# Performance work log

Measured on AMD Instinct MI355X. Metric: run time of the kernel, lower is better.

## Reference

```python
import jax, jax.numpy as jnp
import numpy as np

BIN_AGG = 2  # binAgg in binFunc

def pair_mean(x):
    # mean over non-overlapping groups of BIN_AGG along last dim, then repeat back
    B, C, H, W = x.shape
    m = x.reshape(B, C, H, W // BIN_AGG, BIN_AGG).mean(axis=-1)  # [B,C,H,W/2]
    return jnp.repeat(m, BIN_AGG, axis=-1)  # [B,C,H,W]

def bin_active(x):
    # binFunc(x, abs_bin=True) * sign(x): per-pair mean of |x| carrying the sign of x
    return pair_mean(jnp.abs(x)) * jnp.sign(x)

def setup_inputs() -> dict:
    key = jax.random.key(0)
    k1, k2, k3 = jax.random.split(key, 3)
    Cin, Cout, K = 256, 256, 3
    x = jax.random.normal(k1, (32, Cin, 56, 56), jnp.float32)
    bound = 1.0 / np.sqrt(Cin * K * K)  # torch Conv2d default init range
    weight = jax.random.uniform(k2, (Cout, Cin, K, K), jnp.float32, -bound, bound)
    bias = jax.random.uniform(k3, (Cout,), jnp.float32, -bound, bound)
    return {"x": x, "weight": weight, "bias": bias}

def reference(x, weight, bias):
    xb = bin_active(x)
    out = jax.lax.conv_general_dilated(
        xb, weight, window_strides=(1, 1), padding=[(1, 1), (1, 1)],
        dimension_numbers=("NCHW", "OIHW", "NCHW"))
    return out + bias[None, :, None, None]
```

## Files before the change

kernel.cpp:

```cpp
#include <hip/hip_runtime.h>
#include <hip/hip_bf16.h>
#include <cstdint>

typedef unsigned short u16;
typedef __attribute__((ext_vector_type(8))) short short8;
typedef __attribute__((ext_vector_type(8))) unsigned short ushort8;
typedef __attribute__((ext_vector_type(4))) float f32x4;

#define NB   32
#define CIN  256
#define HH   56
#define WWID 56
#define HP   58
#define WP   58
#define COUT 256
#define NSPAT (NB*HH*WWID)

__device__ __forceinline__ u16 f2bf(float f) {
  uint32_t u = __float_as_uint(f);
  u += 0x7FFFu + ((u >> 16) & 1u);
  return (u16)(u >> 16);
}

__device__ __forceinline__ void gload16(const void* g, void* lds) {
  auto* gp = reinterpret_cast<const __attribute__((address_space(1))) uint32_t*>(
      reinterpret_cast<uintptr_t>(g));
  auto* lp = reinterpret_cast<__attribute__((address_space(3))) uint32_t*>(
      reinterpret_cast<uintptr_t>(lds));
  __builtin_amdgcn_global_load_lds(gp, lp, 16, 0, 0);
}

__global__ __launch_bounds__(256) void prep_x_kernel(const float* __restrict__ x,
                                                     u16* __restrict__ xbp) {
  const int n = blockIdx.x, hp = blockIdx.y, t = threadIdx.x;
  u16* row = xbp + ((size_t)(n*HP + hp))*WP*CIN;
  if (hp == 0 || hp == HP-1) {
    uint32_t* p = (uint32_t*)row;
    for (int i = t; i < WP*CIN/2; i += 256) p[i] = 0;
    return;
  }
  const int h = hp - 1;
  __shared__ u16 lds[HH*CIN];
  if (t < 224) {
    const int f4 = t % 14, cg = t / 14;
    const int sw = f4 & 7;
    #pragma unroll
    for (int it = 0; it < 2; it++) {
      const int c8 = it*16 + cg;
      const int c0 = c8 * 8;
      const float* xc = x + (((size_t)n*CIN + c0)*HH + h)*WWID + f4*4;
      float4 v[8];
      #pragma unroll
      for (int r = 0; r < 8; r++) v[r] = *(const float4*)(xc + (size_t)r*HH*WWID);
      u16 o[8][4];
      #pragma unroll
      for (int r = 0; r < 8; r++) {
        const float m01 = 0.5f*(fabsf(v[r].x)+fabsf(v[r].y));
        const float m23 = 0.5f*(fabsf(v[r].z)+fabsf(v[r].w));
        o[r][0] = f2bf(v[r].x == 0.f ? 0.f : copysignf(m01, v[r].x));
        o[r][1] = f2bf(v[r].y == 0.f ? 0.f : copysignf(m01, v[r].y));
        o[r][2] = f2bf(v[r].z == 0.f ? 0.f : copysignf(m23, v[r].z));
        o[r][3] = f2bf(v[r].w == 0.f ? 0.f : copysignf(m23, v[r].w));
      }
      const int cs = (c8 ^ sw) << 3;
      #pragma unroll
      for (int j = 0; j < 4; j++) {
        ushort8 pk = { o[0][j], o[1][j], o[2][j], o[3][j],
                       o[4][j], o[5][j], o[6][j], o[7][j] };
        *(ushort8*)&lds[(f4*4 + j)*CIN + cs] = pk;
      }
    }
  }
  __syncthreads();
  if (t < 128) ((uint32_t*)row)[t] = 0;
  else ((uint32_t*)(row + (WP-1)*CIN))[t-128] = 0;
  #pragma unroll
  for (int it = 0; it < 7; it++) {
    const int q = it*256 + t;
    const int w = q >> 5, ck = q & 31;
    const short8 v = *(const short8*)&lds[w*CIN + ((ck ^ ((w >> 2) & 7)) << 3)];
    *(short8*)(row + (size_t)(w+1)*CIN + (ck << 3)) = v;
  }
}

__global__ __launch_bounds__(256) void prep_w_kernel(const float* __restrict__ wsrc,
                                                     u16* __restrict__ wr) {
  const int idx = blockIdx.x*256 + threadIdx.x;
  const int co = idx >> 8, ci = idx & 255;
  const float* s = wsrc + (size_t)idx*9;
  #pragma unroll
  for (int p = 0; p < 9; p++)
    wr[((size_t)p*COUT + co)*CIN + ci] = f2bf(s[p]);
}

__global__ __launch_bounds__(256) void conv_kernel(const u16* __restrict__ xbp,
                                                   const u16* __restrict__ wr,
                                                   const float* __restrict__ bias,
                                                   float* __restrict__ out) {
  __shared__ u16 ldsA[3][128*64];
  __shared__ u16 ldsB[3][128*64];
  const int t = threadIdx.x;
  const int wv = t >> 6, l = t & 63;
  const int bid = blockIdx.x;
  const int b9 = (bid & 7)*196 + (bid >> 3);
  const int ntile = b9 & 1, mtile = b9 >> 1;

  const int cs8 = (((l & 7) ^ (l >> 3)) << 3);
  const int rb  = wv*8 + (l >> 3);

  int base0[4];
  #pragma unroll
  for (int i = 0; i < 4; i++) {
    const int m  = mtile*128 + i*32 + rb;
    const int n  = m / 3136, hw = m % 3136;
    base0[i] = ((n*HP + hw/WWID)*WP + (hw%WWID))*CIN;
  }

  auto STAGE = [&](int buf, int ks) {
    const int pos = ks >> 2, cb = ks & 3;
    const int posoff = ((pos/3)*WP + (pos%3))*CIN;
    const int koff = cb*64 + cs8;
    #pragma unroll
    for (int i = 0; i < 4; i++) {
      const u16* gA = wr + (((pos*COUT + ntile*128 + i*32 + rb) << 8) + koff);
      gload16(gA, &ldsA[buf][(i*4 + wv)*512]);
      const u16* gB = xbp + base0[i] + posoff + koff;
      gload16(gB, &ldsB[buf][(i*4 + wv)*512]);
    }
  };

  f32x4 acc[4][4];
  #pragma unroll
  for (int a = 0; a < 4; a++)
    #pragma unroll
    for (int b = 0; b < 4; b++) {
      acc[a][b][0] = 0.f; acc[a][b][1] = 0.f; acc[a][b][2] = 0.f; acc[a][b][3] = 0.f;
    }

  STAGE(0, 0);
  STAGE(1, 1);
  asm volatile("s_waitcnt vmcnt(8)" ::: "memory");
  __builtin_amdgcn_sched_barrier(0);
  __builtin_amdgcn_s_barrier();
  __builtin_amdgcn_sched_barrier(0);

  int cur = 0, nxt = 2;
  #pragma unroll 1
  for (int ks = 0; ks < 36; ks++) {
    if (ks < 34) STAGE(nxt, ks + 2);
    #pragma unroll
    for (int kk = 0; kk < 2; kk++) {
      const int ch = (l >> 4) + 4*kk;
      short8 af[4], bfr[4];
      #pragma unroll
      for (int mi = 0; mi < 4; mi++) {
        const int r = (wv & 1)*64 + mi*16 + (l & 15);
        af[mi] = *(const short8*)&ldsA[cur][r*64 + ((ch ^ (r & 7)) << 3)];
      }
      #pragma unroll
      for (int ni = 0; ni < 4; ni++) {
        const int r = (wv >> 1)*64 + ni*16 + (l & 15);
        bfr[ni] = *(const short8*)&ldsB[cur][r*64 + ((ch ^ (r & 7)) << 3)];
      }
      #pragma unroll
      for (int mi = 0; mi < 4; mi++)
        #pragma unroll
        for (int ni = 0; ni < 4; ni++)
          acc[mi][ni] = __builtin_amdgcn_mfma_f32_16x16x32_bf16(af[mi], bfr[ni], acc[mi][ni], 0, 0, 0);
    }
    if (ks < 35) {
      if (ks < 34) { asm volatile("s_waitcnt vmcnt(8)" ::: "memory"); }
      else         { asm volatile("s_waitcnt vmcnt(0)" ::: "memory"); }
      __builtin_amdgcn_sched_barrier(0);
      __builtin_amdgcn_s_barrier();
      __builtin_amdgcn_sched_barrier(0);
    }
    cur = (cur == 2) ? 0 : cur + 1;
    nxt = (nxt == 2) ? 0 : nxt + 1;
  }

  const int co0 = ntile*128 + (wv & 1)*64 + ((l >> 4) << 2);
  float bi[4][4];
  #pragma unroll
  for (int mi = 0; mi < 4; mi++)
    #pragma unroll
    for (int j = 0; j < 4; j++)
      bi[mi][j] = bias[co0 + mi*16 + j];
  const int mb = mtile*128 + (wv >> 1)*64 + (l & 15);
  #pragma unroll
  for (int ni = 0; ni < 4; ni++) {
    const int m = mb + ni*16;
    const int n = m / 3136, hw = m % 3136;
    float* orow = out + (size_t)n*COUT*3136 + hw;
    #pragma unroll
    for (int mi = 0; mi < 4; mi++) {
      #pragma unroll
      for (int j = 0; j < 4; j++)
        orow[(size_t)(co0 + mi*16 + j)*3136] = acc[mi][ni][j] + bi[mi][j];
    }
  }
}

extern "C" void kernel_launch(void* const* d_in, const int* in_sizes, int n_in,
                              void* d_out, int out_size, void* d_ws, size_t ws_size,
                              hipStream_t stream) {
  const float* x      = (const float*)d_in[0];
  const float* weight = (const float*)d_in[1];
  const float* bias   = (const float*)d_in[2];
  float* out = (float*)d_out;

  u16* xbp = (u16*)d_ws;
  u16* wrr = xbp + (size_t)NB*HP*WP*CIN;

  prep_x_kernel<<<dim3(NB, HP), 256, 0, stream>>>(x, xbp);
  prep_w_kernel<<<dim3(256), 256, 0, stream>>>(weight, wrr);
  conv_kernel<<<dim3(NSPAT/128 * 2), 256, 0, stream>>>(xbp, wrr, bias, out);
}
```

Before: 374.3 us.

## Switch conv main loop to double-buffered LDS with precomputed pointers

The conv kernel's main loop moves from a 3-stage LDS ring with manual vmcnt waits to a 2-stage ping-pong. The loop is unrolled by 4 per filter position, plain __syncthreads handles synchronisation, and the global pointers advance incrementally. Per-lane swizzled LDS read offsets are precomputed once, which removes per-iteration address arithmetic. The smaller LDS footprint may let more workgroups fit per CU. The trade-off is a shorter prefetch distance, and each barrier now drains every outstanding load.

```diff
diff --git a/kernel.cpp b/kernel.cpp
--- a/kernel.cpp
+++ b/kernel.cpp
@@ -97,8 +97,8 @@
                                                    const u16* __restrict__ wr,
                                                    const float* __restrict__ bias,
                                                    float* __restrict__ out) {
-  __shared__ u16 ldsA[3][128*64];
-  __shared__ u16 ldsB[3][128*64];
+  __shared__ u16 ldsA[2][128*64];
+  __shared__ u16 ldsB[2][128*64];
   const int t = threadIdx.x;
   const int wv = t >> 6, l = t & 63;
   const int bid = blockIdx.x;
@@ -108,26 +108,36 @@
   const int cs8 = (((l & 7) ^ (l >> 3)) << 3);
   const int rb  = wv*8 + (l >> 3);
 
-  int base0[4];
-  #pragma unroll
-  for (int i = 0; i < 4; i++) {
-    const int m  = mtile*128 + i*32 + rb;
-    const int n  = m / 3136, hw = m % 3136;
-    base0[i] = ((n*HP + hw/WWID)*WP + (hw%WWID))*CIN;
-  }
-
-  auto STAGE = [&](int buf, int ks) {
-    const int pos = ks >> 2, cb = ks & 3;
-    const int posoff = ((pos/3)*WP + (pos%3))*CIN;
-    const int koff = cb*64 + cs8;
-    #pragma unroll
-    for (int i = 0; i < 4; i++) {
-      const u16* gA = wr + (((pos*COUT + ntile*128 + i*32 + rb) << 8) + koff);
-      gload16(gA, &ldsA[buf][(i*4 + wv)*512]);
-      const u16* gB = xbp + base0[i] + posoff + koff;
-      gload16(gB, &ldsB[buf][(i*4 + wv)*512]);
-    }
-  };
+  const u16* pA0; const u16* pA1; const u16* pA2; const u16* pA3;
+  const u16* pB0; const u16* pB1; const u16* pB2; const u16* pB3;
+  {
+    const int m0 = mtile*128 + 0*32 + rb, m1 = mtile*128 + 1*32 + rb;
+    const int m2 = mtile*128 + 2*32 + rb, m3 = mtile*128 + 3*32 + rb;
+    pA0 = wr + ((ntile*128 + 0*32 + rb) << 8) + cs8;
+    pA1 = wr + ((ntile*128 + 1*32 + rb) << 8) + cs8;
+    pA2 = wr + ((ntile*128 + 2*32 + rb) << 8) + cs8;
+    pA3 = wr + ((ntile*128 + 3*32 + rb) << 8) + cs8;
+    pB0 = xbp + ((m0/3136*HP + (m0%3136)/WWID)*WP + (m0%3136)%WWID)*CIN + cs8;
+    pB1 = xbp + ((m1/3136*HP + (m1%3136)/WWID)*WP + (m1%3136)%WWID)*CIN + cs8;
+    pB2 = xbp + ((m2/3136*HP + (m2%3136)/WWID)*WP + (m2%3136)%WWID)*CIN + cs8;
+    pB3 = xbp + ((m3/3136*HP + (m3%3136)/WWID)*WP + (m3%3136)%WWID)*CIN + cs8;
+  }
+
+  int offA[2][4], offB[2][4];
+  #pragma unroll
+  for (int kk = 0; kk < 2; kk++) {
+    const int ch = (l >> 4) + 4*kk;
+    #pragma unroll
+    for (int mi = 0; mi < 4; mi++) {
+      const int r = (wv & 1)*64 + mi*16 + (l & 15);
+      offA[kk][mi] = r*64 + ((ch ^ (l & 7)) << 3);
+    }
+    #pragma unroll
+    for (int ni = 0; ni < 4; ni++) {
+      const int r = (wv >> 1)*64 + ni*16 + (l & 15);
+      offB[kk][ni] = r*64 + ((ch ^ (l & 7)) << 3);
+    }
+  }
 
   f32x4 acc[4][4];
   #pragma unroll
@@ -137,47 +147,55 @@
       acc[a][b][0] = 0.f; acc[a][b][1] = 0.f; acc[a][b][2] = 0.f; acc[a][b][3] = 0.f;
     }
 
-  STAGE(0, 0);
-  STAGE(1, 1);
-  asm volatile("s_waitcnt vmcnt(8)" ::: "memory");
-  __builtin_amdgcn_sched_barrier(0);
-  __builtin_amdgcn_s_barrier();
-  __builtin_amdgcn_sched_barrier(0);
-
-  int cur = 0, nxt = 2;
+#define STAGE_C(buf, cboff) do {                                  \
+    gload16(pA0 + (cboff), &ldsA[buf][(0*4 + wv)*512]);           \
+    gload16(pB0 + (cboff), &ldsB[buf][(0*4 + wv)*512]);           \
+    gload16(pA1 + (cboff), &ldsA[buf][(1*4 + wv)*512]);           \
+    gload16(pB1 + (cboff), &ldsB[buf][(1*4 + wv)*512]);           \
+    gload16(pA2 + (cboff), &ldsA[buf][(2*4 + wv)*512]);           \
+    gload16(pB2 + (cboff), &ldsB[buf][(2*4 + wv)*512]);           \
+    gload16(pA3 + (cboff), &ldsA[buf][(3*4 + wv)*512]);           \
+    gload16(pB3 + (cboff), &ldsB[buf][(3*4 + wv)*512]);           \
+  } while (0)
+
+#define COMPUTE(buf) do {                                                        \
+    _Pragma("unroll")                                                            \
+    for (int kk = 0; kk < 2; kk++) {                                             \
+      short8 af[4], bfv[4];                                                      \
+      _Pragma("unroll")                                                          \
+      for (int mi = 0; mi < 4; mi++)                                             \
+        af[mi] = *(const short8*)&ldsA[buf][offA[kk][mi]];                       \
+      _Pragma("unroll")                                                          \
+      for (int ni = 0; ni < 4; ni++)                                             \
+        bfv[ni] = *(const short8*)&ldsB[buf][offB[kk][ni]];                      \
+      _Pragma("unroll")                                                          \
+      for (int mi = 0; mi < 4; mi++)                                             \
+        _Pragma("unroll")                                                        \
+        for (int ni = 0; ni < 4; ni++)                                           \
+          acc[mi][ni] = __builtin_amdgcn_mfma_f32_16x16x32_bf16(af[mi], bfv[ni], acc[mi][ni], 0, 0, 0); \
+    }                                                                            \
+  } while (0)
+
+  STAGE_C(0, 0);
+  __syncthreads();
+
   #pragma unroll 1
-  for (int ks = 0; ks < 36; ks++) {
-    if (ks < 34) STAGE(nxt, ks + 2);
-    #pragma unroll
-    for (int kk = 0; kk < 2; kk++) {
-      const int ch = (l >> 4) + 4*kk;
-      short8 af[4], bfr[4];
-      #pragma unroll
-      for (int mi = 0; mi < 4; mi++) {
-        const int r = (wv & 1)*64 + mi*16 + (l & 15);
-        af[mi] = *(const short8*)&ldsA[cur][r*64 + ((ch ^ (r & 7)) << 3)];
-      }
-      #pragma unroll
-      for (int ni = 0; ni < 4; ni++) {
-        const int r = (wv >> 1)*64 + ni*16 + (l & 15);
-        bfr[ni] = *(const short8*)&ldsB[cur][r*64 + ((ch ^ (r & 7)) << 3)];
-      }
-      #pragma unroll
-      for (int mi = 0; mi < 4; mi++)
-        #pragma unroll
-        for (int ni = 0; ni < 4; ni++)
-          acc[mi][ni] = __builtin_amdgcn_mfma_f32_16x16x32_bf16(af[mi], bfr[ni], acc[mi][ni], 0, 0, 0);
-    }
-    if (ks < 35) {
-      if (ks < 34) { asm volatile("s_waitcnt vmcnt(8)" ::: "memory"); }
-      else         { asm volatile("s_waitcnt vmcnt(0)" ::: "memory"); }
-      __builtin_amdgcn_sched_barrier(0);
-      __builtin_amdgcn_s_barrier();
-      __builtin_amdgcn_sched_barrier(0);
-    }
-    cur = (cur == 2) ? 0 : cur + 1;
-    nxt = (nxt == 2) ? 0 : nxt + 1;
-  }
+  for (int pos = 0; pos < 8; pos++) {
+    STAGE_C(1, 64);  COMPUTE(0); __syncthreads();
+    STAGE_C(0, 128); COMPUTE(1); __syncthreads();
+    STAGE_C(1, 192); COMPUTE(0); __syncthreads();
+    const int dB = (pos == 2 || pos == 5) ? (WWID*CIN) : CIN;
+    pA0 += COUT*CIN; pA1 += COUT*CIN; pA2 += COUT*CIN; pA3 += COUT*CIN;
+    pB0 += dB; pB1 += dB; pB2 += dB; pB3 += dB;
+    STAGE_C(0, 0);   COMPUTE(1); __syncthreads();
+  }
+  STAGE_C(1, 64);  COMPUTE(0); __syncthreads();
+  STAGE_C(0, 128); COMPUTE(1); __syncthreads();
+  STAGE_C(1, 192); COMPUTE(0); __syncthreads();
+  COMPUTE(1);
+
+#undef STAGE_C
+#undef COMPUTE
 
   const int co0 = ntile*128 + (wv & 1)*64 + ((l >> 4) << 2);
   float bi[4][4];
```

Result: faster. 313.1 us (-16.3%).
